# Optimization experiments

Hardware: AMD Instinct MI355X
Metric: run time of the kernel (lower is better)

Reference implementation:

```python
import jax, jax.numpy as jnp
import numpy as np

EMBED_DIM = 1024
NUM_HEADS = 16
HEAD_DIM = EMBED_DIM // NUM_HEADS
SEG_LEN = 1024  # all segment_lengths equal, dilation_rate == 1


def setup_inputs() -> dict:
    key = jax.random.key(0)
    k1, k2, k3 = jax.random.split(key, 3)
    B, S, E = 2, 4096, EMBED_DIM
    x = jax.random.normal(k1, (B, S, E), dtype=jnp.float32)
    w_qkv = jax.random.normal(k2, (3 * E, E), dtype=jnp.float32) * (E ** -0.5)
    b_qkv = jnp.zeros((3 * E,), dtype=jnp.float32)
    w_out = jax.random.normal(k3, (E, E), dtype=jnp.float32) * (E ** -0.5)
    b_out = jnp.zeros((E,), dtype=jnp.float32)
    return {"x": x, "w_qkv": w_qkv, "b_qkv": b_qkv, "w_out": w_out, "b_out": b_out}


def reference(x, w_qkv, b_qkv, w_out, b_out):
    B, S, E = x.shape
    H, Dh = NUM_HEADS, HEAD_DIM
    scale = 1.0 / np.sqrt(Dh).astype(np.float32)
    # QKV projection
    qkv = x @ w_qkv.T + b_qkv                      # [B, S, 3E]
    qkv = qkv.reshape(B, S, 3, H, Dh).transpose(2, 0, 3, 1, 4)  # [3, B, H, S, Dh]
    q, k, v = qkv[0], qkv[1], qkv[2]
    # Segments tile the sequence; each query attends only within its segment
    # (block-diagonal attention; online-softmax combine across segments is
    # trivial since the segments are disjoint in the query dimension).
    n = S // SEG_LEN
    q = q.reshape(B, H, n, SEG_LEN, Dh)
    k = k.reshape(B, H, n, SEG_LEN, Dh)
    v = v.reshape(B, H, n, SEG_LEN, Dh)
    scores = jnp.einsum("bhnqd,bhnkd->bhnqk", q, k) * scale
    attn = jax.nn.softmax(scores, axis=-1)
    out = jnp.einsum("bhnqk,bhnkd->bhnqd", attn, v)  # [B, H, n, seg, Dh]
    out = out.reshape(B, H, S, Dh).transpose(0, 2, 1, 3).reshape(B, S, E)
    return out @ w_out.T + b_out
```

## Files before the change

kernel.cpp:

```cpp
#include <hip/hip_runtime.h>

typedef __bf16 bf16x8 __attribute__((ext_vector_type(8)));
typedef float f32x4 __attribute__((ext_vector_type(4)));

#define SL2E 0.18033688011112042f

__device__ __forceinline__ unsigned short f2bf(float f) {
  union { float f; unsigned u; } v; v.f = f;
  unsigned r = v.u + 0x7fffu + ((v.u >> 16) & 1u);
  return (unsigned short)(r >> 16);
}

__device__ __forceinline__ float fast_exp2(float x) {
#if __has_builtin(__builtin_amdgcn_exp2f)
  return __builtin_amdgcn_exp2f(x);
#else
  return exp2f(x);
#endif
}

__device__ __forceinline__ unsigned pack_bf2(float lo, float hi) {
  union { float f; unsigned u; } a, b;
  a.f = lo; b.f = hi;
#if __has_builtin(__builtin_amdgcn_perm)
  return __builtin_amdgcn_perm(b.u + 0x7fffu, a.u + 0x7fffu, 0x07060302u);
#else
  return ((b.u + 0x7fffu) & 0xffff0000u) | ((a.u + 0x7fffu) >> 16);
#endif
}

__device__ __forceinline__ void gload16(const unsigned short* g, unsigned short* l) {
  __builtin_amdgcn_global_load_lds(
      (const __attribute__((address_space(1))) unsigned int*)g,
      (__attribute__((address_space(3))) unsigned int*)l, 16, 0, 0);
}

__global__ __launch_bounds__(256) void f32_to_bf16_all(
    const float* __restrict__ x, const float* __restrict__ wq, const float* __restrict__ wo,
    unsigned short* __restrict__ xb, unsigned short* __restrict__ wqb, unsigned short* __restrict__ wob) {
  int i = blockIdx.x * 256 + threadIdx.x;
  const float* src; unsigned short* dst; int off;
  if (i < 2097152) { src = x; dst = xb; off = i; }
  else if (i < 2883584) { src = wq; dst = wqb; off = i - 2097152; }
  else if (i < 3145728) { src = wo; dst = wob; off = i - 2883584; }
  else return;
  float4 v = ((const float4*)src)[off];
  ushort4 o;
  o.x = f2bf(v.x); o.y = f2bf(v.y); o.z = f2bf(v.z); o.w = f2bf(v.w);
  ((ushort4*)dst)[off] = o;
}

__global__ __launch_bounds__(256) void gemm_qkv(
    const unsigned short* __restrict__ A,
    const unsigned short* __restrict__ Bt,
    const float* __restrict__ bias,
    unsigned short* __restrict__ Qb,
    unsigned short* __restrict__ Kb,
    unsigned short* __restrict__ Vtb) {
  const int K = 1024;
  __shared__ unsigned short As[128 * 40];
  __shared__ unsigned short Bs[128 * 40];
  int tid = threadIdx.x;
  int m0 = blockIdx.x * 128, n0 = blockIdx.y * 128;
  int w = tid >> 6, lane = tid & 63, l15 = lane & 15, quad = lane >> 4;
  int wm = (w & 1) * 64, wn = (w >> 1) * 64;

  f32x4 acc[4][4] = {};

  int c0 = tid, c1 = tid + 256;
  int ra0 = c0 >> 2, ca0 = (c0 & 3) * 8;
  int ra1 = c1 >> 2, ca1 = (c1 & 3) * 8;

  for (int kt = 0; kt < K; kt += 32) {
    __syncthreads();
    uint4 a0 = *(const uint4*)(A + (m0 + ra0) * K + kt + ca0);
    uint4 a1 = *(const uint4*)(A + (m0 + ra1) * K + kt + ca1);
    uint4 b0 = *(const uint4*)(Bt + (n0 + ra0) * K + kt + ca0);
    uint4 b1 = *(const uint4*)(Bt + (n0 + ra1) * K + kt + ca1);
    *(uint4*)(As + ra0 * 40 + ca0) = a0;
    *(uint4*)(As + ra1 * 40 + ca1) = a1;
    *(uint4*)(Bs + ra0 * 40 + ca0) = b0;
    *(uint4*)(Bs + ra1 * 40 + ca1) = b1;
    __syncthreads();
    bf16x8 af[4], bfr[4];
#pragma unroll
    for (int i = 0; i < 4; ++i) af[i] = *(const bf16x8*)(As + (wm + i * 16 + l15) * 40 + quad * 8);
#pragma unroll
    for (int j = 0; j < 4; ++j) bfr[j] = *(const bf16x8*)(Bs + (wn + j * 16 + l15) * 40 + quad * 8);
#pragma unroll
    for (int i = 0; i < 4; ++i)
#pragma unroll
      for (int j = 0; j < 4; ++j)
        acc[i][j] = __builtin_amdgcn_mfma_f32_16x16x32_bf16(af[i], bfr[j], acc[i][j], 0, 0, 0);
  }

  int b = m0 >> 12;
  int sblk = (m0 & 4095) + wm + quad * 4;
#pragma unroll
  for (int j = 0; j < 4; ++j) {
    int n_j = n0 + wn + j * 16 + l15;
    float bv = bias[n_j];
    int t = n_j >> 10, h = (n_j >> 6) & 15, d = n_j & 63;
    if (t == 2) {
      int vbase = ((b * 16 + h) * 64 + d) * 4096;
#pragma unroll
      for (int i = 0; i < 4; ++i) {
        int s = sblk + i * 16;
        ushort4 pk;
        pk.x = f2bf(acc[i][j][0] + bv);
        pk.y = f2bf(acc[i][j][1] + bv);
        pk.z = f2bf(acc[i][j][2] + bv);
        pk.w = f2bf(acc[i][j][3] + bv);
        *(ushort4*)(Vtb + vbase + s) = pk;
      }
    } else {
      unsigned short* dst = (t == 0) ? Qb : Kb;
      float sc = (t == 0) ? SL2E : 1.0f;
      int base = (b * 16 + h) * 4096 * 64 + d;
#pragma unroll
      for (int i = 0; i < 4; ++i)
#pragma unroll
        for (int r = 0; r < 4; ++r) {
          int s = sblk + i * 16 + r;
          dst[base + s * 64] = f2bf((acc[i][j][r] + bv) * sc);
        }
    }
  }
}

#define LDP 72

#define SWZ(r, cg) ((((r) * 8) + ((cg) ^ ((r) & 7))) * 8)

__global__ __launch_bounds__(256) void attn_k(
    const unsigned short* __restrict__ Qb,
    const unsigned short* __restrict__ Kb,
    const unsigned short* __restrict__ Vtb,
    unsigned short* __restrict__ Ab) {
  __shared__ unsigned short KV[2][2][4096];
  __shared__ unsigned short Ps[4][16 * LDP];

  int tid = threadIdx.x;
  int idx = blockIdx.x;
  int grp = idx & 127, qblk = idx >> 7;
  int seg = grp & 3, h = (grp >> 2) & 15, b = grp >> 6;
  int w = tid >> 6, lane = tid & 63, l15 = lane & 15, quad = lane >> 4;
  int bh = b * 16 + h;
  int q0 = seg * 1024 + qblk * 256 + w * 64;

  const unsigned short* Kg = Kb + (bh * 4096 + seg * 1024) * 64;
  const unsigned short* Vg = Vtb + bh * 64 * 4096 + seg * 1024;

  int r0 = w * 16 + (lane >> 3);
  int cs = ((lane & 7) ^ (lane >> 3)) * 8;

  const unsigned short* Qg = Qb + (bh * 4096 + q0) * 64;
  bf16x8 qf[4][2];
#pragma unroll
  for (int qb = 0; qb < 4; ++qb)
#pragma unroll
    for (int kk = 0; kk < 2; ++kk)
      qf[qb][kk] = *(const bf16x8*)(Qg + (qb * 16 + l15) * 64 + kk * 32 + quad * 8);

  f32x4 o[4][4] = {};
  float lsum[4] = {0.f, 0.f, 0.f, 0.f};
  unsigned short* Pw = Ps[w];

  {
    unsigned short* dk = &KV[0][0][w * 1024];
    unsigned short* dv = &KV[0][1][w * 1024];
    gload16(Kg + r0 * 64 + cs, dk);
    gload16(Kg + (r0 + 8) * 64 + cs, dk + 512);
    gload16(Vg + r0 * 4096 + cs, dv);
    gload16(Vg + (r0 + 8) * 4096 + cs, dv + 512);
  }

#pragma unroll 2
  for (int kt = 0; kt < 16; ++kt) {
    int cur = kt & 1;
    __syncthreads();
    if (kt < 15) {
      unsigned short* dk = &KV[cur ^ 1][0][w * 1024];
      unsigned short* dv = &KV[cur ^ 1][1][w * 1024];
      const unsigned short* kN = Kg + (kt + 1) * 4096;
      const unsigned short* vN = Vg + (kt + 1) * 64;
      gload16(kN + r0 * 64 + cs, dk);
      gload16(kN + (r0 + 8) * 64 + cs, dk + 512);
      gload16(vN + r0 * 4096 + cs, dv);
      gload16(vN + (r0 + 8) * 4096 + cs, dv + 512);
    }
    const unsigned short* Kt = KV[cur][0];
    const unsigned short* Vt = KV[cur][1];

    uint2 pp[4][4];
#pragma unroll
    for (int half = 0; half < 2; ++half) {
      f32x4 st[2][4] = {};
#pragma unroll
      for (int kk = 0; kk < 2; ++kk) {
        int cg = kk * 4 + quad;
        bf16x8 kf0 = *(const bf16x8*)(Kt + SWZ(half * 32 + l15, cg));
        bf16x8 kf1 = *(const bf16x8*)(Kt + SWZ(half * 32 + 16 + l15, cg));
#pragma unroll
        for (int qb = 0; qb < 4; ++qb) {
          st[0][qb] = __builtin_amdgcn_mfma_f32_16x16x32_bf16(kf0, qf[qb][kk], st[0][qb], 0, 0, 0);
          st[1][qb] = __builtin_amdgcn_mfma_f32_16x16x32_bf16(kf1, qf[qb][kk], st[1][qb], 0, 0, 0);
        }
      }
#pragma unroll
      for (int kb = 0; kb < 2; ++kb)
#pragma unroll
        for (int qb = 0; qb < 4; ++qb) {
          f32x4 s = st[kb][qb];
          float p0 = fast_exp2(s[0]), p1 = fast_exp2(s[1]);
          float p2 = fast_exp2(s[2]), p3 = fast_exp2(s[3]);
          lsum[qb] += (p0 + p1) + (p2 + p3);
          uint2 d;
          d.x = pack_bf2(p0, p1);
          d.y = pack_bf2(p2, p3);
          pp[qb][half * 2 + kb] = d;
        }
    }

    bf16x8 vf[2][4];
#pragma unroll
    for (int kk = 0; kk < 2; ++kk)
#pragma unroll
      for (int db = 0; db < 4; ++db)
        vf[kk][db] = *(const bf16x8*)(Vt + SWZ(db * 16 + l15, kk * 4 + quad));
#pragma unroll
    for (int qb = 0; qb < 4; ++qb) {
#pragma unroll
      for (int g = 0; g < 4; ++g)
        *(uint2*)(Pw + l15 * LDP + g * 16 + quad * 4) = pp[qb][g];
#pragma unroll
      for (int kk = 0; kk < 2; ++kk) {
        bf16x8 pa = *(const bf16x8*)(Pw + l15 * LDP + kk * 32 + quad * 8);
#pragma unroll
        for (int db = 0; db < 4; ++db)
          o[qb][db] = __builtin_amdgcn_mfma_f32_16x16x32_bf16(pa, vf[kk][db], o[qb][db], 0, 0, 0);
      }
    }
  }

#pragma unroll
  for (int qb = 0; qb < 4; ++qb) {
    lsum[qb] += __shfl_xor(lsum[qb], 16);
    lsum[qb] += __shfl_xor(lsum[qb], 32);
  }

  float* Wf = (float*)(&KV[0][0][0]) + w * 1024;
#pragma unroll
  for (int qb = 0; qb < 4; ++qb) {
#pragma unroll
    for (int db = 0; db < 4; ++db)
#pragma unroll
      for (int r = 0; r < 4; ++r)
        Wf[(quad * 4 + r) * 64 + db * 16 + l15] = o[qb][db][r];
    float inv = 1.0f / lsum[qb];
    float4 x0 = *(float4*)(Wf + l15 * 64 + quad * 8);
    float4 x1 = *(float4*)(Wf + l15 * 64 + quad * 8 + 4);
    float4 x2 = *(float4*)(Wf + l15 * 64 + (quad + 4) * 8);
    float4 x3 = *(float4*)(Wf + l15 * 64 + (quad + 4) * 8 + 4);
    uint4 u0, u1;
    u0.x = pack_bf2(x0.x * inv, x0.y * inv);
    u0.y = pack_bf2(x0.z * inv, x0.w * inv);
    u0.z = pack_bf2(x1.x * inv, x1.y * inv);
    u0.w = pack_bf2(x1.z * inv, x1.w * inv);
    u1.x = pack_bf2(x2.x * inv, x2.y * inv);
    u1.y = pack_bf2(x2.z * inv, x2.w * inv);
    u1.z = pack_bf2(x3.x * inv, x3.y * inv);
    u1.w = pack_bf2(x3.z * inv, x3.w * inv);
    int sg = q0 + qb * 16 + l15;
    int base = (b * 4096 + sg) * 1024 + h * 64;
    *(uint4*)(Ab + base + quad * 8) = u0;
    *(uint4*)(Ab + base + (quad + 4) * 8) = u1;
  }
}

__global__ __launch_bounds__(256) void gemm_out(
    const unsigned short* __restrict__ A,
    const unsigned short* __restrict__ Bt,
    const float* __restrict__ bias,
    float* __restrict__ C) {
  const int K = 1024;
  __shared__ unsigned short As[128 * 40];
  __shared__ unsigned short Bs[128 * 40];
  int tid = threadIdx.x;
  int m0 = blockIdx.x * 128, n0 = blockIdx.y * 128;
  int w = tid >> 6, lane = tid & 63, l15 = lane & 15, quad = lane >> 4;
  int wm = (w & 1) * 64, wn = (w >> 1) * 64;

  f32x4 acc[4][4] = {};

  int c0 = tid, c1 = tid + 256;
  int ra0 = c0 >> 2, ca0 = (c0 & 3) * 8;
  int ra1 = c1 >> 2, ca1 = (c1 & 3) * 8;

  for (int kt = 0; kt < K; kt += 32) {
    __syncthreads();
    uint4 a0 = *(const uint4*)(A + (m0 + ra0) * K + kt + ca0);
    uint4 a1 = *(const uint4*)(A + (m0 + ra1) * K + kt + ca1);
    uint4 b0 = *(const uint4*)(Bt + (n0 + ra0) * K + kt + ca0);
    uint4 b1 = *(const uint4*)(Bt + (n0 + ra1) * K + kt + ca1);
    *(uint4*)(As + ra0 * 40 + ca0) = a0;
    *(uint4*)(As + ra1 * 40 + ca1) = a1;
    *(uint4*)(Bs + ra0 * 40 + ca0) = b0;
    *(uint4*)(Bs + ra1 * 40 + ca1) = b1;
    __syncthreads();
    bf16x8 af[4], bfr[4];
#pragma unroll
    for (int i = 0; i < 4; ++i) af[i] = *(const bf16x8*)(As + (wm + i * 16 + l15) * 40 + quad * 8);
#pragma unroll
    for (int j = 0; j < 4; ++j) bfr[j] = *(const bf16x8*)(Bs + (wn + j * 16 + l15) * 40 + quad * 8);
#pragma unroll
    for (int i = 0; i < 4; ++i)
#pragma unroll
      for (int j = 0; j < 4; ++j)
        acc[i][j] = __builtin_amdgcn_mfma_f32_16x16x32_bf16(af[i], bfr[j], acc[i][j], 0, 0, 0);
  }

#pragma unroll
  for (int j = 0; j < 4; ++j) {
    int n_j = n0 + wn + j * 16 + l15;
    float bv = bias[n_j];
#pragma unroll
    for (int i = 0; i < 4; ++i)
#pragma unroll
      for (int r = 0; r < 4; ++r) {
        int m = m0 + wm + i * 16 + quad * 4 + r;
        C[m * 1024 + n_j] = acc[i][j][r] + bv;
      }
  }
}

extern "C" void kernel_launch(void* const* d_in, const int* in_sizes, int n_in,
                              void* d_out, int out_size, void* d_ws, size_t ws_size,
                              hipStream_t stream) {
  const float* x     = (const float*)d_in[0];
  const float* w_qkv = (const float*)d_in[1];
  const float* b_qkv = (const float*)d_in[2];
  const float* w_out = (const float*)d_in[3];
  const float* b_out = (const float*)d_in[4];
  float* out = (float*)d_out;
  char* ws = (char*)d_ws;

  unsigned short* wqkvb = (unsigned short*)(ws);
  unsigned short* woutb = (unsigned short*)(ws + 6291456);
  unsigned short* Qb    = (unsigned short*)(ws + 8388608);
  unsigned short* Kb    = (unsigned short*)(ws + 25165824);
  unsigned short* Vtb   = (unsigned short*)(ws + 41943040);
  unsigned short* xb    = (unsigned short*)(ws + 58720256);
  unsigned short* Ab    = xb;

  f32_to_bf16_all<<<12288, 256, 0, stream>>>(x, w_qkv, w_out, xb, wqkvb, woutb);
  gemm_qkv<<<dim3(64, 24), 256, 0, stream>>>(xb, wqkvb, b_qkv, Qb, Kb, Vtb);
  attn_k<<<512, 256, 0, stream>>>(Qb, Kb, Vtb, Ab);
  gemm_out<<<dim3(64, 8), 256, 0, stream>>>(Ab, woutb, b_out, out);
}
```

Measured before the change: 259.8 us.

## Use direct global-to-LDS loads with XOR swizzle and BK=64 in both GEMMs

Both projection GEMMs now stage tiles through the existing gload16 helper, which copies global memory straight into LDS without passing through registers. Tiles are stored in an XOR-swizzled layout to avoid bank conflicts. The K-step grows from 32 to 64, which halves the number of barrier pairs per tile. This uses more LDS per block, which may lower occupancy, and there is still no double buffering, so loads and MFMA work do not overlap.

```diff
diff --git a/kernel.cpp b/kernel.cpp
--- a/kernel.cpp
+++ b/kernel.cpp
@@ -50,6 +50,7 @@
   ((ushort4*)dst)[off] = o;
 }
 
+
 __global__ __launch_bounds__(256) void gemm_qkv(
     const unsigned short* __restrict__ A,
     const unsigned short* __restrict__ Bt,
@@ -58,8 +59,8 @@
     unsigned short* __restrict__ Kb,
     unsigned short* __restrict__ Vtb) {
   const int K = 1024;
-  __shared__ unsigned short As[128 * 40];
-  __shared__ unsigned short Bs[128 * 40];
+  __shared__ unsigned short As[128 * 64];
+  __shared__ unsigned short Bs[128 * 64];
   int tid = threadIdx.x;
   int m0 = blockIdx.x * 128, n0 = blockIdx.y * 128;
   int w = tid >> 6, lane = tid & 63, l15 = lane & 15, quad = lane >> 4;
@@ -67,31 +68,35 @@
 
   f32x4 acc[4][4] = {};
 
-  int c0 = tid, c1 = tid + 256;
-  int ra0 = c0 >> 2, ca0 = (c0 & 3) * 8;
-  int ra1 = c1 >> 2, ca1 = (c1 & 3) * 8;
-
-  for (int kt = 0; kt < K; kt += 32) {
-    __syncthreads();
-    uint4 a0 = *(const uint4*)(A + (m0 + ra0) * K + kt + ca0);
-    uint4 a1 = *(const uint4*)(A + (m0 + ra1) * K + kt + ca1);
-    uint4 b0 = *(const uint4*)(Bt + (n0 + ra0) * K + kt + ca0);
-    uint4 b1 = *(const uint4*)(Bt + (n0 + ra1) * K + kt + ca1);
-    *(uint4*)(As + ra0 * 40 + ca0) = a0;
-    *(uint4*)(As + ra1 * 40 + ca1) = a1;
-    *(uint4*)(Bs + ra0 * 40 + ca0) = b0;
-    *(uint4*)(Bs + ra1 * 40 + ca1) = b1;
-    __syncthreads();
-    bf16x8 af[4], bfr[4];
-#pragma unroll
-    for (int i = 0; i < 4; ++i) af[i] = *(const bf16x8*)(As + (wm + i * 16 + l15) * 40 + quad * 8);
-#pragma unroll
-    for (int j = 0; j < 4; ++j) bfr[j] = *(const bf16x8*)(Bs + (wn + j * 16 + l15) * 40 + quad * 8);
-#pragma unroll
-    for (int i = 0; i < 4; ++i)
-#pragma unroll
-      for (int j = 0; j < 4; ++j)
-        acc[i][j] = __builtin_amdgcn_mfma_f32_16x16x32_bf16(af[i], bfr[j], acc[i][j], 0, 0, 0);
+  int rs = w * 32 + (lane >> 3);
+  int cs = ((lane & 7) ^ (lane >> 3)) * 8;
+  const unsigned short* Ag = A + (m0 + rs) * K + cs;
+  const unsigned short* Bg = Bt + (n0 + rs) * K + cs;
+  unsigned short* Asl = As + w * 2048;
+  unsigned short* Bsl = Bs + w * 2048;
+
+  for (int kt = 0; kt < K; kt += 64) {
+    __syncthreads();
+#pragma unroll
+    for (int i = 0; i < 4; ++i) {
+      gload16(Ag + i * 8 * K + kt, Asl + i * 512);
+      gload16(Bg + i * 8 * K + kt, Bsl + i * 512);
+    }
+    __syncthreads();
+#pragma unroll
+    for (int kk = 0; kk < 2; ++kk) {
+      int swk = (((kk * 4 + quad) ^ (l15 & 7))) * 8;
+      bf16x8 af[4], bfr[4];
+#pragma unroll
+      for (int i = 0; i < 4; ++i) af[i] = *(const bf16x8*)(As + (wm + i * 16 + l15) * 64 + swk);
+#pragma unroll
+      for (int j = 0; j < 4; ++j) bfr[j] = *(const bf16x8*)(Bs + (wn + j * 16 + l15) * 64 + swk);
+#pragma unroll
+      for (int i = 0; i < 4; ++i)
+#pragma unroll
+        for (int j = 0; j < 4; ++j)
+          acc[i][j] = __builtin_amdgcn_mfma_f32_16x16x32_bf16(af[i], bfr[j], acc[i][j], 0, 0, 0);
+    }
   }
 
   int b = m0 >> 12;
@@ -129,7 +134,6 @@
 }
 
 #define LDP 72
-
 #define SWZ(r, cg) ((((r) * 8) + ((cg) ^ ((r) & 7))) * 8)
 
 __global__ __launch_bounds__(256) void attn_k(
@@ -284,8 +288,8 @@
     const float* __restrict__ bias,
     float* __restrict__ C) {
   const int K = 1024;
-  __shared__ unsigned short As[128 * 40];
-  __shared__ unsigned short Bs[128 * 40];
+  __shared__ unsigned short As[128 * 64];
+  __shared__ unsigned short Bs[128 * 64];
   int tid = threadIdx.x;
   int m0 = blockIdx.x * 128, n0 = blockIdx.y * 128;
   int w = tid >> 6, lane = tid & 63, l15 = lane & 15, quad = lane >> 4;
@@ -293,31 +297,35 @@
 
   f32x4 acc[4][4] = {};
 
-  int c0 = tid, c1 = tid + 256;
-  int ra0 = c0 >> 2, ca0 = (c0 & 3) * 8;
-  int ra1 = c1 >> 2, ca1 = (c1 & 3) * 8;
-
-  for (int kt = 0; kt < K; kt += 32) {
-    __syncthreads();
-    uint4 a0 = *(const uint4*)(A + (m0 + ra0) * K + kt + ca0);
-    uint4 a1 = *(const uint4*)(A + (m0 + ra1) * K + kt + ca1);
-    uint4 b0 = *(const uint4*)(Bt + (n0 + ra0) * K + kt + ca0);
-    uint4 b1 = *(const uint4*)(Bt + (n0 + ra1) * K + kt + ca1);
-    *(uint4*)(As + ra0 * 40 + ca0) = a0;
-    *(uint4*)(As + ra1 * 40 + ca1) = a1;
-    *(uint4*)(Bs + ra0 * 40 + ca0) = b0;
-    *(uint4*)(Bs + ra1 * 40 + ca1) = b1;
-    __syncthreads();
-    bf16x8 af[4], bfr[4];
-#pragma unroll
-    for (int i = 0; i < 4; ++i) af[i] = *(const bf16x8*)(As + (wm + i * 16 + l15) * 40 + quad * 8);
-#pragma unroll
-    for (int j = 0; j < 4; ++j) bfr[j] = *(const bf16x8*)(Bs + (wn + j * 16 + l15) * 40 + quad * 8);
-#pragma unroll
-    for (int i = 0; i < 4; ++i)
-#pragma unroll
-      for (int j = 0; j < 4; ++j)
-        acc[i][j] = __builtin_amdgcn_mfma_f32_16x16x32_bf16(af[i], bfr[j], acc[i][j], 0, 0, 0);
+  int rs = w * 32 + (lane >> 3);
+  int cs = ((lane & 7) ^ (lane >> 3)) * 8;
+  const unsigned short* Ag = A + (m0 + rs) * K + cs;
+  const unsigned short* Bg = Bt + (n0 + rs) * K + cs;
+  unsigned short* Asl = As + w * 2048;
+  unsigned short* Bsl = Bs + w * 2048;
+
+  for (int kt = 0; kt < K; kt += 64) {
+    __syncthreads();
+#pragma unroll
+    for (int i = 0; i < 4; ++i) {
+      gload16(Ag + i * 8 * K + kt, Asl + i * 512);
+      gload16(Bg + i * 8 * K + kt, Bsl + i * 512);
+    }
+    __syncthreads();
+#pragma unroll
+    for (int kk = 0; kk < 2; ++kk) {
+      int swk = (((kk * 4 + quad) ^ (l15 & 7))) * 8;
+      bf16x8 af[4], bfr[4];
+#pragma unroll
+      for (int i = 0; i < 4; ++i) af[i] = *(const bf16x8*)(As + (wm + i * 16 + l15) * 64 + swk);
+#pragma unroll
+      for (int j = 0; j < 4; ++j) bfr[j] = *(const bf16x8*)(Bs + (wn + j * 16 + l15) * 64 + swk);
+#pragma unroll
+      for (int i = 0; i < 4; ++i)
+#pragma unroll
+        for (int j = 0; j < 4; ++j)
+          acc[i][j] = __builtin_amdgcn_mfma_f32_16x16x32_bf16(af[i], bfr[j], acc[i][j], 0, 0, 0);
+    }
   }
 
 #pragma unroll
```

Measured after the change: 228.8 us. 1.14x faster.
